# Optimization experiments

Hardware: AMD Instinct MI355X
Metric: run time of the kernel (lower is better)

The kernel has to match this reference:

```python
import jax, jax.numpy as jnp
import numpy as np

N_X = 8_388_608      # number of input node values
N_EDGES = 33_554_432 # number of (ptr, csr) edge entries
N_OUT = 8_388_608    # number of output segments = csr[-1] + 1


def setup_inputs() -> dict:
    key = jax.random.key(0)
    k1, k2, k3 = jax.random.split(key, 3)
    x = jax.random.normal(k1, (N_X,), dtype=jnp.float32)
    ptrs = jax.random.randint(k2, (N_EDGES,), 0, N_X, dtype=jnp.int32)
    # csr is a sorted (nondecreasing) segment-id array; force last id to N_OUT-1
    csr = jnp.sort(jax.random.randint(k3, (N_EDGES,), 0, N_OUT, dtype=jnp.int32))
    csr = csr.at[-1].set(N_OUT - 1)
    return {"x": x, "ptrs": ptrs, "csr": csr}


def reference(x, ptrs, csr):
    # output[j] = sum over edges e with csr[e] == j of x[ptrs[e]]
    # Equivalent to torch: zeros(N_OUT).scatter_add(0, csr, x[ptrs]).
    # csr is sorted, so this is a fused gather + segmented reduction.
    src = x[ptrs]  # [N_EDGES]
    return jax.ops.segment_sum(src, csr, num_segments=N_OUT, indices_are_sorted=True)
```

## Files before the change

### kernel.cpp

```cpp
#include <hip/hip_runtime.h>

typedef int      iv4 __attribute__((ext_vector_type(4)));
typedef unsigned uv4 __attribute__((ext_vector_type(4)));

#define NREGS   128
#define RSH     16
#define BLK1    512
#define EPT1    16
#define CHUNK1  (BLK1 * EPT1)
#define CPB     16
#define BLK2    1024
#define CAP     38400

__global__ __launch_bounds__(BLK1) void sort_chunks_kernel(
    const float* __restrict__ x,
    const int*   __restrict__ ptrs,
    const int*   __restrict__ csr,
    float*       __restrict__ out,
    unsigned*    __restrict__ wse,
    int*         __restrict__ wsb,
    long long eb)
{
    __shared__ int      hist[NREGS];
    __shared__ int      bounds[NREGS + 1];
    __shared__ unsigned packed[CHUNK1];

    const int c = blockIdx.x, tid = threadIdx.x;
    const long long base = (long long)c * CHUNK1;
    const int cb = (int)(base / eb);
    const int seg_base = csr[(long long)cb * eb];

    if (tid < NREGS) hist[tid] = 0;
    __syncthreads();

    int ps[EPT1], cs[EPT1];
    const iv4* p4 = reinterpret_cast<const iv4*>(ptrs + base);
    const iv4* s4 = reinterpret_cast<const iv4*>(csr + base);
    #pragma unroll
    for (int q = 0; q < EPT1 / 4; ++q) {
        iv4 p = __builtin_nontemporal_load(p4 + q * BLK1 + tid);
        ps[q*4+0] = p[0]; ps[q*4+1] = p[1]; ps[q*4+2] = p[2]; ps[q*4+3] = p[3];
    }
    #pragma unroll
    for (int q = 0; q < EPT1 / 4; ++q) {
        iv4 s = __builtin_nontemporal_load(s4 + q * BLK1 + tid);
        cs[q*4+0] = s[0]; cs[q*4+1] = s[1]; cs[q*4+2] = s[2]; cs[q*4+3] = s[3];
    }

    #pragma unroll
    for (int i = 0; i < EPT1; ++i) atomicAdd(&hist[ps[i] >> RSH], 1);
    __syncthreads();
    if (tid == 0) {
        int acc = 0;
        #pragma unroll
        for (int r = 0; r < NREGS; ++r) { bounds[r] = acc; acc += hist[r]; }
        bounds[NREGS] = acc;
    }
    __syncthreads();
    if (tid < NREGS) hist[tid] = bounds[tid];
    __syncthreads();

    #pragma unroll
    for (int i = 0; i < EPT1; ++i) {
        int pp = ps[i], ss = cs[i];
        int r  = pp >> RSH;
        int sl = ss - seg_base;
        unsigned pk;
        if (sl >= 0xFFFF) {
            atomicAdd(out + ss, x[pp]);
            pk = (((unsigned)pp & 0xFFFFu) << 16) | 0xFFFFu;
        } else {
            pk = (((unsigned)pp & 0xFFFFu) << 16) | (unsigned)sl;
        }
        int pos = atomicAdd(&hist[r], 1);
        packed[pos] = pk;
    }
    __syncthreads();

    {
        const uv4* pl = reinterpret_cast<const uv4*>(packed);
        uv4* w4 = reinterpret_cast<uv4*>(wse + base);
        for (int i = tid; i < CHUNK1 / 4; i += BLK1)
            __builtin_nontemporal_store(pl[i], w4 + i);
    }
    for (int i = tid; i <= NREGS; i += BLK1)
        wsb[(size_t)c * (NREGS + 1) + i] = bounds[i];
}

__global__ __launch_bounds__(BLK2) void consume_kernel(
    const float*    __restrict__ x,
    const int*      __restrict__ csr,
    float*          __restrict__ out,
    const unsigned* __restrict__ wse,
    const int*      __restrict__ wsb,
    long long eb)
{
    __shared__ float accum[CAP];
    __shared__ int   cbnd[CPB][NREGS + 1];

    const int c = blockIdx.x, tid = threadIdx.x;
    const int w = tid >> 6, lane = tid & 63;
    const long long base = (long long)c * eb;

    for (int i = tid; i < CAP; i += BLK2) accum[i] = 0.f;
    {
        const int* src = wsb + (size_t)c * CPB * (NREGS + 1);
        for (int i = tid; i < CPB * (NREGS + 1); i += BLK2)
            (&cbnd[0][0])[i] = src[i];
    }
    const int seg_base = csr[base];
    const int seg_last = csr[base + eb - 1];
    __syncthreads();

    const long long chunk_base = base + (long long)w * CHUNK1;
    for (int r = 0; r < NREGS; ++r) {
        const int lo = cbnd[w][r], hi = cbnd[w][r + 1];
        const int rb = r << RSH;
        for (int i = lo + lane; i < hi; i += 64) {
            unsigned pk = __builtin_nontemporal_load(wse + chunk_base + i);
            float val = x[rb | (int)(pk >> 16)];
            int   sl  = (int)(pk & 0xFFFFu);
            if (sl == 0xFFFF) continue;
            if (sl < CAP) atomicAdd(&accum[sl], val);
            else          atomicAdd(out + seg_base + sl, val);
        }
    }
    __syncthreads();

    const int range = seg_last - seg_base + 1;
    const int hi = range < CAP ? range : CAP;
    for (int i = tid; i < hi; i += BLK2) {
        float v = accum[i];
        if (i == 0 || i == range - 1) {
            if (v != 0.f) atomicAdd(out + seg_base + i, v);
        } else {
            out[seg_base + i] = v;
        }
    }
}

#define EPT   16
#define BLK   256
#define CHUNK (BLK * EPT)
#define NREG  16
#define SW(s) ((s) ^ (((s) >> 4) & 0xF))

__global__ __launch_bounds__(BLK, 4) void seg_gather_sort_kernel(
    const float* __restrict__ x,
    const int*   __restrict__ ptrs,
    const int*   __restrict__ csr,
    float*       __restrict__ out,
    int n_edges, int rshift, int n_chunks)
{
    __shared__ int      hist[NREG];
    __shared__ int      bounds[NREG + 1];
    __shared__ unsigned packed[CHUNK];
    __shared__ float    vlds[CHUNK];

    const int tid = threadIdx.x;
    const unsigned lmask = (1u << rshift) - 1u;

    for (int c = blockIdx.x; c < n_chunks; c += gridDim.x) {
        const long long base_e = (long long)c * CHUNK;
        if (base_e + CHUNK <= n_edges) {
            const long long e0 = base_e + (long long)tid * EPT;
            const iv4* p4 = reinterpret_cast<const iv4*>(ptrs + e0);
            const iv4* c4 = reinterpret_cast<const iv4*>(csr + e0);
            int ps[EPT], cs[EPT];
            #pragma unroll
            for (int q = 0; q < EPT / 4; ++q) {
                iv4 p = __builtin_nontemporal_load(p4 + q);
                ps[q*4+0] = p[0]; ps[q*4+1] = p[1]; ps[q*4+2] = p[2]; ps[q*4+3] = p[3];
            }
            #pragma unroll
            for (int q = 0; q < EPT / 4; ++q) {
                iv4 cc = __builtin_nontemporal_load(c4 + q);
                cs[q*4+0] = cc[0]; cs[q*4+1] = cc[1]; cs[q*4+2] = cc[2]; cs[q*4+3] = cc[3];
            }
            if (tid < NREG) hist[tid] = 0;
            __syncthreads();
            #pragma unroll
            for (int i = 0; i < EPT; ++i) atomicAdd(&hist[ps[i] >> rshift], 1);
            __syncthreads();
            if (tid == 0) {
                int acc = 0; bounds[0] = 0;
                #pragma unroll
                for (int r = 0; r < NREG; ++r) { acc += hist[r]; bounds[r+1] = acc; }
                #pragma unroll
                for (int r = 0; r < NREG; ++r) hist[r] = bounds[r];
            }
            __syncthreads();
            #pragma unroll
            for (int i = 0; i < EPT; ++i) {
                int r   = ps[i] >> rshift;
                int pos = atomicAdd(&hist[r], 1);
                packed[pos] = (((unsigned)ps[i] & lmask) << 12) | (unsigned)(tid*EPT+i);
            }
            __syncthreads();
            {
                int r = 0;
                #pragma unroll
                for (int k = 0; k < EPT; ++k) {
                    int e = k * BLK + tid;
                    while (e >= bounds[r + 1]) ++r;
                    unsigned pk = packed[e];
                    int ptr  = (r << rshift) | (int)(pk >> 12);
                    int slot = (int)(pk & 0xFFFu);
                    vlds[SW(slot)] = x[ptr];
                }
            }
            __syncthreads();
            float v[EPT];
            #pragma unroll
            for (int i = 0; i < EPT; ++i) v[i] = vlds[SW(tid * EPT + i)];
            int cur = cs[0]; float sum = 0.f; bool first = true;
            #pragma unroll
            for (int i = 0; i < EPT; ++i) {
                int seg = cs[i];
                if (seg != cur) {
                    if (first) { atomicAdd(out + cur, sum); first = false; }
                    else       { out[cur] = sum; }
                    cur = seg; sum = 0.f;
                }
                sum += v[i];
            }
            atomicAdd(out + cur, sum);
            __syncthreads();
        } else {
            long long e0 = base_e + (long long)tid * EPT;
            if (e0 < n_edges) {
                long long eend = e0 + EPT; if (eend > n_edges) eend = n_edges;
                int cur = csr[e0]; float sum = 0.f; bool first = true;
                for (long long e = e0; e < eend; ++e) {
                    int seg = csr[e];
                    if (seg != cur) {
                        if (first) { atomicAdd(out + cur, sum); first = false; }
                        else       { out[cur] = sum; }
                        cur = seg; sum = 0.f;
                    }
                    sum += x[ptrs[e]];
                }
                atomicAdd(out + cur, sum);
            }
        }
    }
}

extern "C" void kernel_launch(void* const* d_in, const int* in_sizes, int n_in,
                              void* d_out, int out_size, void* d_ws, size_t ws_size,
                              hipStream_t stream) {
    const float* x    = (const float*)d_in[0];
    const int*   ptrs = (const int*)d_in[1];
    const int*   csr  = (const int*)d_in[2];
    float*       out  = (float*)d_out;

    const int n_x     = in_sizes[0];
    const int n_edges = in_sizes[2];

    (void)hipMemsetAsync(out, 0, (size_t)out_size * sizeof(float), stream);

    const long long eb = (long long)CHUNK1 * CPB;
    const int n_chunks1 = (int)(n_edges / CHUNK1);
    const size_t ws_need = (size_t)n_edges * 4 +
                           (size_t)n_chunks1 * (NREGS + 1) * 4;
    const bool v7_ok = (n_edges % eb == 0) &&
                       (n_x <= (NREGS << RSH)) &&
                       (ws_size >= ws_need);

    if (v7_ok) {
        unsigned* wse = (unsigned*)d_ws;
        int*      wsb = (int*)d_ws + n_edges;
        const int g2  = (int)(n_edges / eb);
        sort_chunks_kernel<<<n_chunks1, BLK1, 0, stream>>>(
            x, ptrs, csr, out, wse, wsb, eb);
        consume_kernel<<<g2, BLK2, 0, stream>>>(
            x, csr, out, wse, wsb, eb);
    } else {
        int rshift = 0;
        while ((1LL << rshift) < (n_x + NREG - 1) / NREG) ++rshift;
        const int n_chunks = (int)(((long long)n_edges + CHUNK - 1) / CHUNK);
        int grid = 1024; if (grid > n_chunks) grid = n_chunks;
        seg_gather_sort_kernel<<<grid, BLK, 0, stream>>>(
            x, ptrs, csr, out, n_edges, rshift, n_chunks);
    }
}
```

Measured before the change: 315.2 us.

## Emit per-edge region bytes so consume kernel reads a flat edge stream

The sort kernel now also writes one byte per edge holding its x-region index, obtained by a binary search over the chunk's region bounds. A new consume kernel streams the packed edges and region bytes linearly, eight per lane, and no longer reconstructs regions from per-chunk bound tables. This removes the bound-table bookkeeping and irregular per-region iteration from the consume phase. The cost is an extra byte per edge of workspace traffic, written once and read once.

```diff
diff --git a/kernel.cpp b/kernel.cpp
--- a/kernel.cpp
+++ b/kernel.cpp
@@ -17,8 +17,9 @@
     const int*   __restrict__ ptrs,
     const int*   __restrict__ csr,
     float*       __restrict__ out,
-    unsigned*    __restrict__ wse,
-    int*         __restrict__ wsb,
+    unsigned*       __restrict__ wse,
+    unsigned char*  __restrict__ wsr,
+    int*            __restrict__ wsb,
     long long eb)
 {
     __shared__ int      hist[NREGS];
@@ -83,8 +84,89 @@
         for (int i = tid; i < CHUNK1 / 4; i += BLK1)
             __builtin_nontemporal_store(pl[i], w4 + i);
     }
+    if (wsr) {
+        const int s0 = tid * EPT1;
+        int lo = 0, hi = NREGS;
+        while (hi - lo > 1) {
+            int mid = (lo + hi) >> 1;
+            if (bounds[mid] <= s0) lo = mid; else hi = mid;
+        }
+        int r = lo;
+        union { unsigned char b[16]; uv4 v; } rbuf;
+        #pragma unroll
+        for (int i = 0; i < EPT1; ++i) {
+            while (bounds[r + 1] <= s0 + i) ++r;
+            rbuf.b[i] = (unsigned char)r;
+        }
+        __builtin_nontemporal_store(rbuf.v,
+            reinterpret_cast<uv4*>(wsr + base + s0));
+    }
     for (int i = tid; i <= NREGS; i += BLK1)
         wsb[(size_t)c * (NREGS + 1) + i] = bounds[i];
+}
+
+__global__ __launch_bounds__(BLK2) void consume_flat_kernel(
+    const float*         __restrict__ x,
+    const int*           __restrict__ csr,
+    float*               __restrict__ out,
+    const unsigned*      __restrict__ wse,
+    const unsigned char* __restrict__ wsr,
+    long long eb)
+{
+    __shared__ float accum[CAP];
+
+    const int c = blockIdx.x, tid = threadIdx.x;
+    const int w = tid >> 6, lane = tid & 63;
+    const long long base = (long long)c * eb;
+
+    for (int i = tid; i < CAP; i += BLK2) accum[i] = 0.f;
+    const int seg_base = csr[base];
+    const int seg_last = csr[base + eb - 1];
+    __syncthreads();
+
+    const long long cbase = base + (long long)w * CHUNK1;
+    const uv4*      pk4 = reinterpret_cast<const uv4*>(wse + cbase);
+    const unsigned* r4  = reinterpret_cast<const unsigned*>(wsr + cbase);
+
+    for (int k = 0; k < CHUNK1 / (64 * 8); ++k) {
+        const int e = k * 512 + lane * 8;
+        uv4 a = __builtin_nontemporal_load(pk4 + (e >> 2));
+        uv4 b = __builtin_nontemporal_load(pk4 + (e >> 2) + 1);
+        unsigned ra = __builtin_nontemporal_load(r4 + (e >> 2));
+        unsigned rb = __builtin_nontemporal_load(r4 + (e >> 2) + 1);
+
+        unsigned pk[8] = { a[0], a[1], a[2], a[3], b[0], b[1], b[2], b[3] };
+        int rg[8];
+        #pragma unroll
+        for (int j = 0; j < 4; ++j) rg[j]     = (int)((ra >> (8 * j)) & 0xFFu);
+        #pragma unroll
+        for (int j = 0; j < 4; ++j) rg[4 + j] = (int)((rb >> (8 * j)) & 0xFFu);
+
+        float v[8];
+        #pragma unroll
+        for (int j = 0; j < 8; ++j)
+            v[j] = x[(rg[j] << RSH) | (int)(pk[j] >> 16)];
+
+        #pragma unroll
+        for (int j = 0; j < 8; ++j) {
+            int sl = (int)(pk[j] & 0xFFFFu);
+            if (sl == 0xFFFF) continue;
+            if (sl < CAP) atomicAdd(&accum[sl], v[j]);
+            else          atomicAdd(out + seg_base + sl, v[j]);
+        }
+    }
+    __syncthreads();
+
+    const int range = seg_last - seg_base + 1;
+    const int hi = range < CAP ? range : CAP;
+    for (int i = tid; i < hi; i += BLK2) {
+        float v = accum[i];
+        if (i == 0 || i == range - 1) {
+            if (v != 0.f) atomicAdd(out + seg_base + i, v);
+        } else {
+            out[seg_base + i] = v;
+        }
+    }
 }
 
 __global__ __launch_bounds__(BLK2) void consume_kernel(
@@ -261,18 +343,26 @@
 
     const long long eb = (long long)CHUNK1 * CPB;
     const int n_chunks1 = (int)(n_edges / CHUNK1);
-    const size_t ws_need = (size_t)n_edges * 4 +
-                           (size_t)n_chunks1 * (NREGS + 1) * 4;
-    const bool v7_ok = (n_edges % eb == 0) &&
-                       (n_x <= (NREGS << RSH)) &&
-                       (ws_size >= ws_need);
-
-    if (v7_ok) {
+    const size_t bounds_bytes = (size_t)n_chunks1 * (NREGS + 1) * 4;
+    const size_t ws_need_v7 = (size_t)n_edges * 4 + bounds_bytes;
+    const size_t ws_need_v8 = (size_t)n_edges * 5 + bounds_bytes;
+    const bool shape_ok = (n_edges % eb == 0) && (n_x <= (NREGS << RSH));
+
+    if (shape_ok && ws_size >= ws_need_v8) {
+        unsigned*      wse = (unsigned*)d_ws;
+        unsigned char* wsr = (unsigned char*)d_ws + (size_t)n_edges * 4;
+        int*           wsb = (int*)(void*)((char*)d_ws + (size_t)n_edges * 5);
+        const int g2 = (int)(n_edges / eb);
+        sort_chunks_kernel<<<n_chunks1, BLK1, 0, stream>>>(
+            x, ptrs, csr, out, wse, wsr, wsb, eb);
+        consume_flat_kernel<<<g2, BLK2, 0, stream>>>(
+            x, csr, out, wse, wsr, eb);
+    } else if (shape_ok && ws_size >= ws_need_v7) {
         unsigned* wse = (unsigned*)d_ws;
         int*      wsb = (int*)d_ws + n_edges;
-        const int g2  = (int)(n_edges / eb);
+        const int g2 = (int)(n_edges / eb);
         sort_chunks_kernel<<<n_chunks1, BLK1, 0, stream>>>(
-            x, ptrs, csr, out, wse, wsb, eb);
+            x, ptrs, csr, out, wse, (unsigned char*)nullptr, wsb, eb);
         consume_kernel<<<g2, BLK2, 0, stream>>>(
             x, csr, out, wse, wsb, eb);
     } else {
```

Result: slower. 431.7 us (+37.0%).

## Split gather into region-local LDS gather kernel and separate segmented reduce kernel

Applied to the files above, without the earlier changes.

Replaces the two-kernel sort/consume pipeline with three kernels. Chunks are now bucketed into 256 regions of 32K x values and stored as separate 16-bit pointer and segment streams. A region-per-block kernel then loads its x slice into LDS and gathers values into a float workspace. A reduce kernel streams the segment ids and values into an LDS accumulator. This trades an extra launch and an extra 32M-float workspace round trip for coalesced, LDS-resident gathers, but only 256 blocks run the gather stage, which may underuse the GPU.

```diff
diff --git a/kernel.cpp b/kernel.cpp
--- a/kernel.cpp
+++ b/kernel.cpp
@@ -2,15 +2,187 @@
 
 typedef int      iv4 __attribute__((ext_vector_type(4)));
 typedef unsigned uv4 __attribute__((ext_vector_type(4)));
-
-#define NREGS   128
-#define RSH     16
+typedef float    fv4 __attribute__((ext_vector_type(4)));
+
+#define NREGS2  256
+#define RSH2    15
+#define REGW    (1 << RSH2)
 #define BLK1    512
 #define EPT1    16
 #define CHUNK1  (BLK1 * EPT1)
 #define CPB     16
 #define BLK2    1024
 #define CAP     38400
+
+__global__ __launch_bounds__(BLK1) void sort_chunks2_kernel(
+    const float* __restrict__ x,
+    const int*   __restrict__ ptrs,
+    const int*   __restrict__ csr,
+    float*       __restrict__ out,
+    unsigned short* __restrict__ wsp,
+    unsigned short* __restrict__ wss,
+    int*            __restrict__ wsb,
+    long long eb)
+{
+    __shared__ int      hist[NREGS2];
+    __shared__ int      scan[NREGS2];
+    __shared__ int      bounds[NREGS2 + 1];
+    __shared__ unsigned packed[CHUNK1];
+
+    const int c = blockIdx.x, tid = threadIdx.x;
+    const long long base = (long long)c * CHUNK1;
+    const int cb = (int)(base / eb);
+    const int seg_base = csr[(long long)cb * eb];
+
+    if (tid < NREGS2) hist[tid] = 0;
+    __syncthreads();
+
+    int ps[EPT1], cs[EPT1];
+    const iv4* p4 = reinterpret_cast<const iv4*>(ptrs + base);
+    const iv4* s4 = reinterpret_cast<const iv4*>(csr + base);
+    #pragma unroll
+    for (int q = 0; q < EPT1 / 4; ++q) {
+        iv4 p = __builtin_nontemporal_load(p4 + q * BLK1 + tid);
+        ps[q*4+0] = p[0]; ps[q*4+1] = p[1]; ps[q*4+2] = p[2]; ps[q*4+3] = p[3];
+    }
+    #pragma unroll
+    for (int q = 0; q < EPT1 / 4; ++q) {
+        iv4 s = __builtin_nontemporal_load(s4 + q * BLK1 + tid);
+        cs[q*4+0] = s[0]; cs[q*4+1] = s[1]; cs[q*4+2] = s[2]; cs[q*4+3] = s[3];
+    }
+
+    #pragma unroll
+    for (int i = 0; i < EPT1; ++i) atomicAdd(&hist[ps[i] >> RSH2], 1);
+    __syncthreads();
+
+    if (tid < NREGS2) scan[tid] = hist[tid];
+    __syncthreads();
+    for (int off = 1; off < NREGS2; off <<= 1) {
+        int v = 0;
+        if (tid < NREGS2) { v = scan[tid]; if (tid >= off) v += scan[tid - off]; }
+        __syncthreads();
+        if (tid < NREGS2) scan[tid] = v;
+        __syncthreads();
+    }
+    if (tid < NREGS2) bounds[tid + 1] = scan[tid];
+    if (tid == 0) bounds[0] = 0;
+    __syncthreads();
+    if (tid < NREGS2) hist[tid] = bounds[tid];
+    __syncthreads();
+
+    #pragma unroll
+    for (int i = 0; i < EPT1; ++i) {
+        int pp = ps[i], ss = cs[i];
+        int r  = pp >> RSH2;
+        int sl = ss - seg_base;
+        unsigned pk;
+        if (sl >= 0xFFFF) {
+            atomicAdd(out + ss, x[pp]);
+            pk = (((unsigned)pp & (REGW - 1)) << 16) | 0xFFFFu;
+        } else {
+            pk = (((unsigned)pp & (REGW - 1)) << 16) | (unsigned)sl;
+        }
+        int pos = atomicAdd(&hist[r], 1);
+        packed[pos] = pk;
+    }
+    __syncthreads();
+
+    {
+        unsigned* p32 = reinterpret_cast<unsigned*>(wsp + base);
+        unsigned* s32 = reinterpret_cast<unsigned*>(wss + base);
+        for (int i = tid; i < CHUNK1 / 2; i += BLK1) {
+            unsigned a = packed[2 * i], b = packed[2 * i + 1];
+            __builtin_nontemporal_store((b & 0xFFFF0000u) | (a >> 16), p32 + i);
+            __builtin_nontemporal_store((b << 16) | (a & 0xFFFFu),     s32 + i);
+        }
+    }
+    for (int i = tid; i <= NREGS2; i += BLK1)
+        wsb[(size_t)c * (NREGS2 + 1) + i] = bounds[i];
+}
+
+__global__ __launch_bounds__(BLK2) void region_gather_kernel(
+    const float*          __restrict__ x,
+    const unsigned short* __restrict__ wsp,
+    float*                __restrict__ wsv,
+    const int*            __restrict__ wsb,
+    int n_chunks, int n_x)
+{
+    __shared__ float xr[REGW];
+
+    const int r = blockIdx.x, tid = threadIdx.x;
+    const int w = tid >> 6, lane = tid & 63;
+    const long long rb = (long long)r << RSH2;
+
+    {
+        const fv4* xs = reinterpret_cast<const fv4*>(x + rb);
+        fv4* xd = reinterpret_cast<fv4*>(xr);
+        for (int i = tid; i < REGW / 4; i += BLK2)
+            if (rb + (long long)i * 4 < n_x) xd[i] = xs[i];
+    }
+    __syncthreads();
+
+    for (int c = w; c < n_chunks; c += CPB) {
+        const int* bc = wsb + (size_t)c * (NREGS2 + 1) + r;
+        const int lo = bc[0], hi = bc[1];
+        const long long cbase = (long long)c * CHUNK1;
+        for (int i = lo + lane; i < hi; i += 64) {
+            unsigned short pl = wsp[cbase + i];
+            wsv[cbase + i] = xr[pl];
+        }
+    }
+}
+
+__global__ __launch_bounds__(BLK2) void reduce_kernel(
+    const int*            __restrict__ csr,
+    float*                __restrict__ out,
+    const unsigned short* __restrict__ wss,
+    const float*          __restrict__ wsv,
+    long long eb)
+{
+    __shared__ float accum[CAP];
+
+    const int c = blockIdx.x, tid = threadIdx.x;
+    const long long base = (long long)c * eb;
+
+    for (int i = tid; i < CAP; i += BLK2) accum[i] = 0.f;
+    const int seg_base = csr[base];
+    const int seg_last = csr[base + eb - 1];
+    __syncthreads();
+
+    const unsigned* s32 = reinterpret_cast<const unsigned*>(wss + base);
+    const fv4*      v4  = reinterpret_cast<const fv4*>(wsv + base);
+    const int iters = (int)(eb / (BLK2 * 8));
+    for (int k = 0; k < iters; ++k) {
+        const int idx = k * BLK2 + tid;
+        uv4 sv = __builtin_nontemporal_load(
+                     reinterpret_cast<const uv4*>(s32) + idx);
+        fv4 va = __builtin_nontemporal_load(v4 + 2 * idx);
+        fv4 vb = __builtin_nontemporal_load(v4 + 2 * idx + 1);
+        #pragma unroll
+        for (int j = 0; j < 8; ++j) {
+            int   sl = (int)((sv[j >> 1] >> (16 * (j & 1))) & 0xFFFFu);
+            float vl = (j < 4) ? va[j] : vb[j - 4];
+            if (sl == 0xFFFF) continue;
+            if (sl < CAP) atomicAdd(&accum[sl], vl);
+            else          atomicAdd(out + seg_base + sl, vl);
+        }
+    }
+    __syncthreads();
+
+    const int range = seg_last - seg_base + 1;
+    const int hi = range < CAP ? range : CAP;
+    for (int i = tid; i < hi; i += BLK2) {
+        float v = accum[i];
+        if (i == 0 || i == range - 1) {
+            if (v != 0.f) atomicAdd(out + seg_base + i, v);
+        } else {
+            out[seg_base + i] = v;
+        }
+    }
+}
+
+#define NREGS   128
+#define RSH     16
 
 __global__ __launch_bounds__(BLK1) void sort_chunks_kernel(
     const float* __restrict__ x,
@@ -46,7 +218,6 @@
         iv4 s = __builtin_nontemporal_load(s4 + q * BLK1 + tid);
         cs[q*4+0] = s[0]; cs[q*4+1] = s[1]; cs[q*4+2] = s[2]; cs[q*4+3] = s[3];
     }
-
     #pragma unroll
     for (int i = 0; i < EPT1; ++i) atomicAdd(&hist[ps[i] >> RSH], 1);
     __syncthreads();
@@ -59,7 +230,6 @@
     __syncthreads();
     if (tid < NREGS) hist[tid] = bounds[tid];
     __syncthreads();
-
     #pragma unroll
     for (int i = 0; i < EPT1; ++i) {
         int pp = ps[i], ss = cs[i];
@@ -76,7 +246,6 @@
         packed[pos] = pk;
     }
     __syncthreads();
-
     {
         const uv4* pl = reinterpret_cast<const uv4*>(packed);
         uv4* w4 = reinterpret_cast<uv4*>(wse + base);
@@ -260,17 +429,32 @@
     (void)hipMemsetAsync(out, 0, (size_t)out_size * sizeof(float), stream);
 
     const long long eb = (long long)CHUNK1 * CPB;
-    const int n_chunks1 = (int)(n_edges / CHUNK1);
-    const size_t ws_need = (size_t)n_edges * 4 +
-                           (size_t)n_chunks1 * (NREGS + 1) * 4;
-    const bool v7_ok = (n_edges % eb == 0) &&
-                       (n_x <= (NREGS << RSH)) &&
-                       (ws_size >= ws_need);
-
-    if (v7_ok) {
+    const int n_chunks1 = n_edges / CHUNK1;
+
+    const size_t wsb9_off  = (size_t)n_edges * 8;
+    const size_t ws_need9  = wsb9_off + (size_t)n_chunks1 * (NREGS2 + 1) * 4;
+    const bool shape_ok9 = (n_edges % eb == 0) && (n_x % 4 == 0) &&
+                           (n_x <= (NREGS2 << RSH2));
+    const size_t ws_need7 = (size_t)n_edges * 4 +
+                            (size_t)n_chunks1 * (NREGS + 1) * 4;
+    const bool shape_ok7 = (n_edges % eb == 0) && (n_x <= (NREGS << RSH));
+
+    if (shape_ok9 && ws_size >= ws_need9) {
+        unsigned short* wsp = (unsigned short*)d_ws;
+        unsigned short* wss = (unsigned short*)d_ws + n_edges;
+        float*          wsv = (float*)(void*)((char*)d_ws + (size_t)n_edges * 4);
+        int*            wsb = (int*)(void*)((char*)d_ws + wsb9_off);
+        const int g2 = (int)(n_edges / eb);
+        sort_chunks2_kernel<<<n_chunks1, BLK1, 0, stream>>>(
+            x, ptrs, csr, out, wsp, wss, wsb, eb);
+        region_gather_kernel<<<NREGS2, BLK2, 0, stream>>>(
+            x, wsp, wsv, wsb, n_chunks1, n_x);
+        reduce_kernel<<<g2, BLK2, 0, stream>>>(
+            csr, out, wss, wsv, eb);
+    } else if (shape_ok7 && ws_size >= ws_need7) {
         unsigned* wse = (unsigned*)d_ws;
         int*      wsb = (int*)d_ws + n_edges;
-        const int g2  = (int)(n_edges / eb);
+        const int g2 = (int)(n_edges / eb);
         sort_chunks_kernel<<<n_chunks1, BLK1, 0, stream>>>(
             x, ptrs, csr, out, wse, wsb, eb);
         consume_kernel<<<g2, BLK2, 0, stream>>>(
```

After: 506.8 us. +60.8%, slower.

## Add three-pass sort/region-gather/invert pipeline staging x regions in LDS

Applied to the files above, without the earlier changes.

Adds a new default path that buckets each 32K-edge chunk's pointers by 256 x-regions, then has one block per region load its 32K-float slice of x into LDS and serve all gathers for that region from shared memory. It then scatters the gathered values back to original edge order in LDS and does the segmented reduction. The goal is to turn random global gathers of x into LDS reads. The cost is extra workspace traffic (packed indices plus gathered values written and reread) and only 256 blocks in the gather pass, which could underuse the GPU.

```diff
diff --git a/kernel.cpp b/kernel.cpp
--- a/kernel.cpp
+++ b/kernel.cpp
@@ -2,15 +2,180 @@
 
 typedef int      iv4 __attribute__((ext_vector_type(4)));
 typedef unsigned uv4 __attribute__((ext_vector_type(4)));
-
-#define NREGS   128
-#define RSH     16
+typedef float    fv4 __attribute__((ext_vector_type(4)));
+
+#define NREGS2  256
+#define RSH2    15
+#define REGW    (1 << RSH2)
+#define CHUNKB  32768
+#define BLKB    1024
+#define EPTB    32
+#define MAXC    1024
+#define SWZ(i)  ((i) ^ (((i) >> 5) & 31))
+
+__global__ __launch_bounds__(BLKB) void sortbig_kernel(
+    const int* __restrict__ ptrs,
+    unsigned*  __restrict__ wse,
+    int*       __restrict__ wsb)
+{
+    __shared__ int      hist[NREGS2];
+    __shared__ int      scn[NREGS2];
+    __shared__ int      bounds[NREGS2 + 1];
+    __shared__ unsigned packed[CHUNKB];
+
+    const int c = blockIdx.x, tid = threadIdx.x;
+    const long long base = (long long)c * CHUNKB;
+
+    if (tid < NREGS2) hist[tid] = 0;
+    __syncthreads();
+
+    int ps[EPTB];
+    const iv4* p4 = reinterpret_cast<const iv4*>(ptrs + base);
+    #pragma unroll
+    for (int q = 0; q < EPTB / 4; ++q) {
+        iv4 p = __builtin_nontemporal_load(p4 + q * BLKB + tid);
+        ps[q*4+0] = p[0]; ps[q*4+1] = p[1]; ps[q*4+2] = p[2]; ps[q*4+3] = p[3];
+    }
+
+    #pragma unroll
+    for (int i = 0; i < EPTB; ++i) atomicAdd(&hist[ps[i] >> RSH2], 1);
+    __syncthreads();
+
+    if (tid < NREGS2) scn[tid] = hist[tid];
+    __syncthreads();
+    for (int off = 1; off < NREGS2; off <<= 1) {
+        int v = 0;
+        if (tid < NREGS2) { v = scn[tid]; if (tid >= off) v += scn[tid - off]; }
+        __syncthreads();
+        if (tid < NREGS2) scn[tid] = v;
+        __syncthreads();
+    }
+    if (tid < NREGS2) bounds[tid + 1] = scn[tid];
+    if (tid == 0) bounds[0] = 0;
+    __syncthreads();
+    if (tid < NREGS2) hist[tid] = bounds[tid];
+    __syncthreads();
+
+    #pragma unroll
+    for (int q = 0; q < EPTB / 4; ++q) {
+        #pragma unroll
+        for (int k = 0; k < 4; ++k) {
+            int pp   = ps[q * 4 + k];
+            int orig = (q << 12) + (tid << 2) + k;
+            int pos  = atomicAdd(&hist[pp >> RSH2], 1);
+            packed[pos] = (((unsigned)pp & (REGW - 1)) << 16) | (unsigned)orig;
+        }
+    }
+    __syncthreads();
+
+    {
+        const uv4* pl = reinterpret_cast<const uv4*>(packed);
+        uv4* w4 = reinterpret_cast<uv4*>(wse + base);
+        for (int i = tid; i < CHUNKB / 4; i += BLKB)
+            __builtin_nontemporal_store(pl[i], w4 + i);
+    }
+    for (int i = tid; i <= NREGS2; i += BLKB)
+        wsb[(size_t)c * (NREGS2 + 1) + i] = bounds[i];
+}
+
+__global__ __launch_bounds__(BLKB) void region_gather2_kernel(
+    const float*    __restrict__ x,
+    const unsigned* __restrict__ wse,
+    float*          __restrict__ wsv,
+    const int*      __restrict__ wsb,
+    int n_chunks, int n_x)
+{
+    __shared__ float xr[REGW];
+    __shared__ int   blo[MAXC];
+    __shared__ int   bhi[MAXC];
+
+    const int r = blockIdx.x, tid = threadIdx.x;
+    const int w = tid >> 6, lane = tid & 63;
+    const long long rb = (long long)r << RSH2;
+
+    {
+        const fv4* xs = reinterpret_cast<const fv4*>(x + rb);
+        fv4* xd = reinterpret_cast<fv4*>(xr);
+        for (int i = tid; i < REGW / 4; i += BLKB)
+            if (rb + (long long)(i + 1) * 4 <= n_x) xd[i] = xs[i];
+    }
+    for (int c = tid; c < n_chunks; c += BLKB) {
+        blo[c] = wsb[(size_t)c * (NREGS2 + 1) + r];
+        bhi[c] = wsb[(size_t)c * (NREGS2 + 1) + r + 1];
+    }
+    __syncthreads();
+
+    for (int c = w; c < n_chunks; c += 16) {
+        const int lo = blo[c], hi = bhi[c];
+        const long long cb = (long long)c * CHUNKB;
+        for (int i = lo + lane; i < hi; i += 64) {
+            unsigned pk = __builtin_nontemporal_load(wse + cb + i);
+            __builtin_nontemporal_store(xr[pk >> 16], wsv + cb + i);
+        }
+    }
+}
+
+__global__ __launch_bounds__(BLKB) void invert_reduce_kernel(
+    const int*      __restrict__ csr,
+    float*          __restrict__ out,
+    const unsigned* __restrict__ wse,
+    const float*    __restrict__ wsv)
+{
+    __shared__ float vlds[CHUNKB];
+
+    const int c = blockIdx.x, tid = threadIdx.x;
+    const long long base = (long long)c * CHUNKB;
+
+    {
+        const uv4* e4 = reinterpret_cast<const uv4*>(wse + base);
+        const fv4* v4 = reinterpret_cast<const fv4*>(wsv + base);
+        for (int i = tid; i < CHUNKB / 4; i += BLKB) {
+            uv4 pk = __builtin_nontemporal_load(e4 + i);
+            fv4 vv = __builtin_nontemporal_load(v4 + i);
+            #pragma unroll
+            for (int k = 0; k < 4; ++k) {
+                int o = (int)(pk[k] & 0xFFFFu);
+                vlds[SWZ(o)] = vv[k];
+            }
+        }
+    }
+    __syncthreads();
+
+    {
+        const int o0 = tid * EPTB;
+        int cs[EPTB];
+        const iv4* s4 = reinterpret_cast<const iv4*>(csr + base + o0);
+        #pragma unroll
+        for (int q = 0; q < EPTB / 4; ++q) {
+            iv4 s = __builtin_nontemporal_load(s4 + q);
+            cs[q*4+0] = s[0]; cs[q*4+1] = s[1]; cs[q*4+2] = s[2]; cs[q*4+3] = s[3];
+        }
+        int   cur   = cs[0];
+        float sum   = 0.f;
+        bool  first = true;
+        #pragma unroll
+        for (int i = 0; i < EPTB; ++i) {
+            int seg = cs[i];
+            if (seg != cur) {
+                if (first) { atomicAdd(out + cur, sum); first = false; }
+                else       { out[cur] = sum; }
+                cur = seg;
+                sum = 0.f;
+            }
+            sum += vlds[SWZ(o0 + i)];
+        }
+        atomicAdd(out + cur, sum);
+    }
+}
+
 #define BLK1    512
 #define EPT1    16
 #define CHUNK1  (BLK1 * EPT1)
 #define CPB     16
 #define BLK2    1024
 #define CAP     38400
+#define NREGS   128
+#define RSH     16
 
 __global__ __launch_bounds__(BLK1) void sort_chunks_kernel(
     const float* __restrict__ x,
@@ -46,7 +211,6 @@
         iv4 s = __builtin_nontemporal_load(s4 + q * BLK1 + tid);
         cs[q*4+0] = s[0]; cs[q*4+1] = s[1]; cs[q*4+2] = s[2]; cs[q*4+3] = s[3];
     }
-
     #pragma unroll
     for (int i = 0; i < EPT1; ++i) atomicAdd(&hist[ps[i] >> RSH], 1);
     __syncthreads();
@@ -59,7 +223,6 @@
     __syncthreads();
     if (tid < NREGS) hist[tid] = bounds[tid];
     __syncthreads();
-
     #pragma unroll
     for (int i = 0; i < EPT1; ++i) {
         int pp = ps[i], ss = cs[i];
@@ -76,7 +239,6 @@
         packed[pos] = pk;
     }
     __syncthreads();
-
     {
         const uv4* pl = reinterpret_cast<const uv4*>(packed);
         uv4* w4 = reinterpret_cast<uv4*>(wse + base);
@@ -143,7 +305,7 @@
 #define BLK   256
 #define CHUNK (BLK * EPT)
 #define NREG  16
-#define SW(s) ((s) ^ (((s) >> 4) & 0xF))
+#define SW5(s) ((s) ^ (((s) >> 4) & 0xF))
 
 __global__ __launch_bounds__(BLK, 4) void seg_gather_sort_kernel(
     const float* __restrict__ x,
@@ -206,13 +368,13 @@
                     unsigned pk = packed[e];
                     int ptr  = (r << rshift) | (int)(pk >> 12);
                     int slot = (int)(pk & 0xFFFu);
-                    vlds[SW(slot)] = x[ptr];
+                    vlds[SW5(slot)] = x[ptr];
                 }
             }
             __syncthreads();
             float v[EPT];
             #pragma unroll
-            for (int i = 0; i < EPT; ++i) v[i] = vlds[SW(tid * EPT + i)];
+            for (int i = 0; i < EPT; ++i) v[i] = vlds[SW5(tid * EPT + i)];
             int cur = cs[0]; float sum = 0.f; bool first = true;
             #pragma unroll
             for (int i = 0; i < EPT; ++i) {
@@ -259,22 +421,37 @@
 
     (void)hipMemsetAsync(out, 0, (size_t)out_size * sizeof(float), stream);
 
-    const long long eb = (long long)CHUNK1 * CPB;
-    const int n_chunks1 = (int)(n_edges / CHUNK1);
-    const size_t ws_need = (size_t)n_edges * 4 +
-                           (size_t)n_chunks1 * (NREGS + 1) * 4;
-    const bool v7_ok = (n_edges % eb == 0) &&
-                       (n_x <= (NREGS << RSH)) &&
-                       (ws_size >= ws_need);
-
-    if (v7_ok) {
+    const int n_chunksB = n_edges / CHUNKB;
+    const size_t need10 = (size_t)n_edges * 8 +
+                          (size_t)n_chunksB * (NREGS2 + 1) * 4;
+    const bool ok10 = (n_edges % CHUNKB == 0) && (n_chunksB <= MAXC) &&
+                      (n_x % 4 == 0) && (n_x <= (NREGS2 << RSH2)) &&
+                      (ws_size >= need10);
+
+    const long long eb7 = (long long)CHUNK1 * CPB;
+    const int n_chunks1 = n_edges / CHUNK1;
+    const size_t need7 = (size_t)n_edges * 4 +
+                         (size_t)n_chunks1 * (NREGS + 1) * 4;
+    const bool ok7 = (n_edges % eb7 == 0) && (n_x <= (NREGS << RSH)) &&
+                     (ws_size >= need7);
+
+    if (ok10) {
+        unsigned* wse = (unsigned*)d_ws;
+        float*    wsv = (float*)(void*)((char*)d_ws + (size_t)n_edges * 4);
+        int*      wsb = (int*)(void*)((char*)d_ws + (size_t)n_edges * 8);
+        sortbig_kernel<<<n_chunksB, BLKB, 0, stream>>>(ptrs, wse, wsb);
+        region_gather2_kernel<<<NREGS2, BLKB, 0, stream>>>(
+            x, wse, wsv, wsb, n_chunksB, n_x);
+        invert_reduce_kernel<<<n_chunksB, BLKB, 0, stream>>>(
+            csr, out, wse, wsv);
+    } else if (ok7) {
         unsigned* wse = (unsigned*)d_ws;
         int*      wsb = (int*)d_ws + n_edges;
-        const int g2  = (int)(n_edges / eb);
+        const int g2 = (int)(n_edges / eb7);
         sort_chunks_kernel<<<n_chunks1, BLK1, 0, stream>>>(
-            x, ptrs, csr, out, wse, wsb, eb);
+            x, ptrs, csr, out, wse, wsb, eb7);
         consume_kernel<<<g2, BLK2, 0, stream>>>(
-            x, csr, out, wse, wsb, eb);
+            x, csr, out, wse, wsb, eb7);
     } else {
         int rshift = 0;
         while ((1LL << rshift) < (n_x + NREG - 1) / NREG) ++rshift;
```

Result: slower. 433.7 us (+37.6%).
